# Kernel tuning notes

Measured on AMD Instinct MI355X. Metric: run time of the kernel, lower is better.

## Reference

```python
import jax, jax.numpy as jnp
import numpy as np

N, E, H, NUM_RBF = 50000, 800000, 32, 32
D_IN = 2 * (NUM_RBF + H)  # 128: att_src(H) + att_dst(H) + rbf(2*NUM_RBF)
LN_EPS = 1e-5


def _decompose(t):
    # irreducible decomposition of [..., 3, 3] tensor
    eye = jnp.eye(3, dtype=t.dtype)
    I = jnp.mean(jnp.diagonal(t, axis1=-2, axis2=-1), axis=-1)[..., None, None] * eye
    A = 0.5 * (t - jnp.swapaxes(t, -1, -2))
    S = 0.5 * (t + jnp.swapaxes(t, -1, -2)) - I
    return I, A, S


def _tnorm(t):
    # squared Frobenius norm over last two dims -> [..., H]
    return (t ** 2).sum((-2, -1))


def _chan_lin(t, W):
    # nn.Linear over channel dim: t [N,H,3,3], W [H_out,H_in]
    return jnp.einsum('nhij,gh->ngij', t, W)


def setup_inputs() -> dict:
    key = jax.random.key(0)
    ks = jax.random.split(key, 12)

    def lin(k, o, i):
        return (jax.random.normal(k, (o, i), jnp.float32) / np.sqrt(i)).astype(jnp.float32)

    return {
        'X': jax.random.normal(ks[0], (N, H, 3, 3), jnp.float32),
        'rbf': jax.random.normal(ks[1], (E, 2 * NUM_RBF), jnp.float32),
        'dist': jax.random.uniform(ks[2], (E,), jnp.float32),
        'src': jax.random.randint(ks[3], (E,), 0, N),
        'dst': jax.random.randint(ks[4], (E,), 0, N),
        'Ws0': lin(ks[5], H, D_IN), 'b0': jnp.zeros((H,), jnp.float32),
        'Ws1': lin(ks[6], 2 * H, H), 'b1': jnp.zeros((2 * H,), jnp.float32),
        'Ws2': lin(ks[7], 3 * H, 2 * H), 'b2': jnp.zeros((3 * H,), jnp.float32),
        'Wt': (jax.random.normal(ks[8], (6, H, H), jnp.float32) / np.sqrt(H)).astype(jnp.float32),
        'ln_w': jnp.ones((3 * H,), jnp.float32), 'ln_b': jnp.zeros((3 * H,), jnp.float32),
        'lin_w': lin(ks[9], H, 3 * H), 'lin_b': jnp.zeros((H,), jnp.float32),
    }


def reference(X, rbf, dist, src, dst, Ws0, b0, Ws1, b1, Ws2, b2, Wt, ln_w, ln_b, lin_w, lin_b):
    n = X.shape[0]
    act = jax.nn.silu

    # atom_inf branch: per-node scalar attributes from tensor norms
    I, A, S = _decompose(X)
    x = jnp.concatenate([_tnorm(I), _tnorm(A), _tnorm(S)], axis=-1)  # [N, 3H]
    mu = x.mean(-1, keepdims=True)
    var = x.var(-1, keepdims=True)
    x = (x - mu) / jnp.sqrt(var + LN_EPS) * ln_w + ln_b
    att = act(x @ lin_w.T + lin_b)  # [N, H]

    # edge features: cat(att[src], att[dst], rbf) -> scalar MLP
    e = jnp.concatenate([att[src], att[dst], rbf], axis=-1)  # [E, D_IN]
    e = act(e @ Ws0.T + b0)
    e = act(e @ Ws1.T + b1)
    e = act(e @ Ws2.T + b2)  # [E, 3H]
    C = jnp.ones_like(dist)  # original code overwrites cutoff with ones
    e = (e * C[:, None]).reshape(e.shape[0], H, 3)  # [E, H, 3]

    # normalize node tensors, decompose, per-channel linear mix
    Xn = X / (_tnorm(X) + 1.0)[..., None, None]
    I, A, S = _decompose(Xn)
    I = _chan_lin(I, Wt[0])
    A = _chan_lin(A, Wt[1])
    S = _chan_lin(S, Wt[2])
    Y = I + A + S

    # tensor message passing: gather src, scale by edge factor, scatter-sum to dst
    def mp(T, f):
        return jax.ops.segment_sum(T[src] * f[:, :, None, None], dst, num_segments=n)

    msg = mp(I, e[..., 0]) + mp(A, e[..., 1]) + mp(S, e[..., 2])

    # O(3) group
    B1 = jnp.matmul(msg, Y)
    B2 = jnp.matmul(Y, msg)
    I, A, S = _decompose(B1 + B2)

    normp1 = (_tnorm(I + A + S) + 1.0)[..., None, None]
    I, A, S = I / normp1, A / normp1, S / normp1
    I = _chan_lin(I, Wt[3])
    A = _chan_lin(A, Wt[4])
    S = _chan_lin(S, Wt[5])
    dX = I + A + S
    X_out = Xn + dX + jnp.matmul(dX, dX)  # matrix_power(dX, 2)
    return X_out, e
```

## Files before the change

kernel.cpp:

```cpp
#include <hip/hip_runtime.h>
#include <math.h>

#define HC 32
#define NODE_PER_BLK 8

typedef _Float16 half8 __attribute__((ext_vector_type(8)));
typedef float float4v __attribute__((ext_vector_type(4)));

__device__ __forceinline__ float silu_f(float x) { return x / (1.0f + __expf(-x)); }

__device__ __forceinline__ unsigned int pk2(float a, float b) {
    union { _Float16 h[2]; unsigned int u; } t;
    t.h[0] = (_Float16)a; t.h[1] = (_Float16)b;
    return t.u;
}
__device__ __forceinline__ void unpk2(unsigned int u, float& a, float& b) {
    union { unsigned int u; _Float16 h[2]; } t;
    t.u = u;
    a = (float)t.h[0]; b = (float)t.h[1];
}

__device__ __forceinline__ void recon3(const float* c, float* T) {
    T[0] = c[0] + c[4];  T[1] = c[1] + c[5];  T[2] = c[2] + c[6];
    T[3] = -c[1] + c[5]; T[4] = c[0] + c[7];  T[5] = c[3] + c[8];
    T[6] = -c[2] + c[6]; T[7] = -c[3] + c[8]; T[8] = c[0] - c[4] - c[7];
}

__global__ void prep_weights(const float* __restrict__ Ws0, const float* __restrict__ Ws1,
                             const float* __restrict__ Ws2,
                             _Float16* __restrict__ wf1, _Float16* __restrict__ wf2,
                             _Float16* __restrict__ wf3) {
    int t = blockIdx.x * 256 + threadIdx.x;
    int j = t & 7;
    int lane = (t >> 3) & 63;
    int q = lane >> 4, r = lane & 15;
    if (t < 4096) {
        int fi = t >> 9, kt = fi >> 1, nt = fi & 1;
        wf1[t] = (_Float16)Ws0[(16 * nt + r) * 128 + 32 * kt + 8 * q + j];
    } else if (t < 6144) {
        int t2 = t - 4096;
        int nt = t2 >> 9;
        wf2[t2] = (_Float16)Ws1[(16 * nt + r) * 32 + 8 * q + j];
    } else if (t < 12288) {
        int t3 = t - 6144;
        int fi = t3 >> 9, kt = fi / 6, nt = fi % 6;
        wf3[t3] = (_Float16)Ws2[(16 * nt + r) * 64 + 32 * kt + 8 * q + j];
    }
}

__global__ void hist_kernel(const int* __restrict__ dst, int* __restrict__ cnt, int E) {
    int e = blockIdx.x * 256 + threadIdx.x;
    if (e < E) atomicAdd(&cnt[dst[e]], 1);
}

__global__ __launch_bounds__(1024) void scan_a(const int* __restrict__ cnt,
                                               int* __restrict__ bsum, int N) {
    __shared__ int s[1024];
    int i = blockIdx.x * 1024 + threadIdx.x;
    s[threadIdx.x] = (i < N) ? cnt[i] : 0;
    __syncthreads();
    #pragma unroll
    for (int o = 512; o; o >>= 1) {
        if (threadIdx.x < o) s[threadIdx.x] += s[threadIdx.x + o];
        __syncthreads();
    }
    if (threadIdx.x == 0) bsum[blockIdx.x] = s[0];
}

__global__ __launch_bounds__(1024) void scan_b(int* __restrict__ bsum, int nb) {
    __shared__ int s[1024];
    int v = (threadIdx.x < nb) ? bsum[threadIdx.x] : 0;
    s[threadIdx.x] = v;
    __syncthreads();
    #pragma unroll
    for (int o = 1; o < 1024; o <<= 1) {
        int t = (threadIdx.x >= o) ? s[threadIdx.x - o] : 0;
        __syncthreads();
        s[threadIdx.x] += t;
        __syncthreads();
    }
    if (threadIdx.x < nb) bsum[threadIdx.x] = s[threadIdx.x] - v;
}

__global__ __launch_bounds__(1024) void scan_c(const int* __restrict__ cnt,
                                               const int* __restrict__ bsum,
                                               int* __restrict__ off,
                                               int* __restrict__ cursor, int N) {
    __shared__ int s[1024];
    int i = blockIdx.x * 1024 + threadIdx.x;
    int v = (i < N) ? cnt[i] : 0;
    s[threadIdx.x] = v;
    __syncthreads();
    #pragma unroll
    for (int o = 1; o < 1024; o <<= 1) {
        int t = (threadIdx.x >= o) ? s[threadIdx.x - o] : 0;
        __syncthreads();
        s[threadIdx.x] += t;
        __syncthreads();
    }
    int ex = bsum[blockIdx.x] + s[threadIdx.x] - v;
    if (i < N) {
        off[i] = ex;
        cursor[i] = ex;
        if (i == N - 1) off[N] = ex + v;
    }
}

__global__ void scatter_kernel(const int* __restrict__ src, const int* __restrict__ dst,
                               int* __restrict__ cursor, int2* __restrict__ elist, int E) {
    int e = blockIdx.x * 256 + threadIdx.x;
    if (e >= E) return;
    int d = dst[e];
    int pos = atomicAdd(&cursor[d], 1);
    elist[pos] = make_int2(e, src[e]);
}

__global__ void node_prep(const float* __restrict__ X,
                          const float* __restrict__ lin_w, const float* __restrict__ lin_b,
                          const float* __restrict__ ln_w, const float* __restrict__ ln_b,
                          const float* __restrict__ Wt,
                          float* __restrict__ att, unsigned int* __restrict__ comp_g, int N) {
    __shared__ float sX[NODE_PER_BLK][96];
    __shared__ float sC[NODE_PER_BLK][HC * 9];
    int grp = threadIdx.x >> 5;
    int lane = threadIdx.x & 31;
    int n = blockIdx.x * NODE_PER_BLK + grp;
    bool valid = (n < N);

    float m = 0, a01 = 0, a02 = 0, a12 = 0, s00 = 0, s01 = 0, s02 = 0, s11 = 0, s12 = 0, s22 = 0;
    float tI = 0, tA = 0, tS = 0, tX = 0;
    if (valid) {
        const float* xp = X + (size_t)n * 288 + lane * 9;
        float t00 = xp[0], t01 = xp[1], t02 = xp[2];
        float t10 = xp[3], t11 = xp[4], t12 = xp[5];
        float t20 = xp[6], t21 = xp[7], t22 = xp[8];
        m = (t00 + t11 + t22) * (1.0f / 3.0f);
        a01 = 0.5f * (t01 - t10); a02 = 0.5f * (t02 - t20); a12 = 0.5f * (t12 - t21);
        s00 = t00 - m; s11 = t11 - m; s22 = t22 - m;
        s01 = 0.5f * (t01 + t10); s02 = 0.5f * (t02 + t20); s12 = 0.5f * (t12 + t21);
        tI = 3.0f * m * m;
        tA = 2.0f * (a01 * a01 + a02 * a02 + a12 * a12);
        tS = s00 * s00 + s11 * s11 + s22 * s22 + 2.0f * (s01 * s01 + s02 * s02 + s12 * s12);
        tX = tI + tA + tS;
    }
    float lsum = tI + tA + tS;
    #pragma unroll
    for (int o = 16; o; o >>= 1) lsum += __shfl_xor(lsum, o, 32);
    float mu = lsum * (1.0f / 96.0f);
    float d0 = tI - mu, d1 = tA - mu, d2 = tS - mu;
    float lsq = d0 * d0 + d1 * d1 + d2 * d2;
    #pragma unroll
    for (int o = 16; o; o >>= 1) lsq += __shfl_xor(lsq, o, 32);
    float rstd = rsqrtf(lsq * (1.0f / 96.0f) + 1e-5f);
    if (valid) {
        sX[grp][lane]      = d0 * rstd * ln_w[lane]      + ln_b[lane];
        sX[grp][32 + lane] = d1 * rstd * ln_w[32 + lane] + ln_b[32 + lane];
        sX[grp][64 + lane] = d2 * rstd * ln_w[64 + lane] + ln_b[64 + lane];
    }
    __syncthreads();
    if (valid) {
        float acc = lin_b[lane];
        const float* wr = lin_w + lane * 96;
        #pragma unroll
        for (int k = 0; k < 96; k++) acc += wr[k] * sX[grp][k];
        att[(size_t)n * 32 + lane] = silu_f(acc);
        float inv = 1.0f / (tX + 1.0f);
        float* cc = &sC[grp][lane * 9];
        cc[0] = m * inv;
        cc[1] = a01 * inv; cc[2] = a02 * inv; cc[3] = a12 * inv;
        cc[4] = s00 * inv; cc[5] = s01 * inv; cc[6] = s02 * inv;
        cc[7] = s11 * inv; cc[8] = s12 * inv;
    }
    __syncthreads();
    if (valid) {
        float o[9];
        #pragma unroll
        for (int c = 0; c < 9; c++) o[c] = 0.0f;
        const float* w0 = Wt + lane * 32;
        const float* w1 = Wt + 1024 + lane * 32;
        const float* w2 = Wt + 2048 + lane * 32;
        #pragma unroll
        for (int h = 0; h < 32; h++) {
            float wi = w0[h], wa = w1[h], ws = w2[h];
            const float* ch = &sC[grp][h * 9];
            o[0] += wi * ch[0];
            o[1] += wa * ch[1]; o[2] += wa * ch[2]; o[3] += wa * ch[3];
            o[4] += ws * ch[4]; o[5] += ws * ch[5]; o[6] += ws * ch[6];
            o[7] += ws * ch[7]; o[8] += ws * ch[8];
        }
        unsigned int* cgp = comp_g + (size_t)n * 160 + lane;
        cgp[0]   = pk2(o[0], o[1]);
        cgp[32]  = pk2(o[2], o[3]);
        cgp[64]  = pk2(o[4], o[5]);
        cgp[96]  = pk2(o[6], o[7]);
        cgp[128] = pk2(o[8], 0.0f);
    }
}

__device__ __forceinline__ half8 cvt8v(const float* p) {
    float4 v0 = ((const float4*)p)[0];
    float4 v1 = ((const float4*)p)[1];
    half8 h;
    h[0] = (_Float16)v0.x; h[1] = (_Float16)v0.y; h[2] = (_Float16)v0.z; h[3] = (_Float16)v0.w;
    h[4] = (_Float16)v1.x; h[5] = (_Float16)v1.y; h[6] = (_Float16)v1.z; h[7] = (_Float16)v1.w;
    return h;
}

__global__ __launch_bounds__(256) void edge_mfma(
    const float* __restrict__ att, const float* __restrict__ rbf,
    const int* __restrict__ src, const int* __restrict__ dst,
    const _Float16* __restrict__ wf1, const _Float16* __restrict__ wf2,
    const _Float16* __restrict__ wf3,
    const float* __restrict__ b0, const float* __restrict__ b1, const float* __restrict__ b2,
    float* __restrict__ e_out, int E) {
    __shared__ _Float16 hbuf[4][16][72];
    int w = threadIdx.x >> 6;
    int lane = threadIdx.x & 63;
    int q = lane >> 4, r = lane & 15;
    int ebase = blockIdx.x * 64 + w * 16;
    int er = min(ebase + r, E - 1);
    int s = src[er], d = dst[er];

    half8 a0 = cvt8v(att + (size_t)s * 32 + 8 * q);
    half8 a1 = cvt8v(att + (size_t)d * 32 + 8 * q);
    half8 a2 = cvt8v(rbf + (size_t)er * 64 + 8 * q);
    half8 a3 = cvt8v(rbf + (size_t)er * 64 + 32 + 8 * q);

    const half8* W1 = (const half8*)wf1;
    float bn0 = b0[r], bn1 = b0[16 + r];
    float4v acc10 = {bn0, bn0, bn0, bn0};
    float4v acc11 = {bn1, bn1, bn1, bn1};
    acc10 = __builtin_amdgcn_mfma_f32_16x16x32_f16(a0, W1[0 * 64 + lane], acc10, 0, 0, 0);
    acc11 = __builtin_amdgcn_mfma_f32_16x16x32_f16(a0, W1[1 * 64 + lane], acc11, 0, 0, 0);
    acc10 = __builtin_amdgcn_mfma_f32_16x16x32_f16(a1, W1[2 * 64 + lane], acc10, 0, 0, 0);
    acc11 = __builtin_amdgcn_mfma_f32_16x16x32_f16(a1, W1[3 * 64 + lane], acc11, 0, 0, 0);
    acc10 = __builtin_amdgcn_mfma_f32_16x16x32_f16(a2, W1[4 * 64 + lane], acc10, 0, 0, 0);
    acc11 = __builtin_amdgcn_mfma_f32_16x16x32_f16(a2, W1[5 * 64 + lane], acc11, 0, 0, 0);
    acc10 = __builtin_amdgcn_mfma_f32_16x16x32_f16(a3, W1[6 * 64 + lane], acc10, 0, 0, 0);
    acc11 = __builtin_amdgcn_mfma_f32_16x16x32_f16(a3, W1[7 * 64 + lane], acc11, 0, 0, 0);
    #pragma unroll
    for (int reg = 0; reg < 4; reg++) {
        hbuf[w][4 * q + reg][r]      = (_Float16)silu_f(acc10[reg]);
        hbuf[w][4 * q + reg][16 + r] = (_Float16)silu_f(acc11[reg]);
    }

    half8 ah1 = *(const half8*)&hbuf[w][r][8 * q];
    const half8* W2 = (const half8*)wf2;
    float4v acc2[4];
    #pragma unroll
    for (int nt = 0; nt < 4; nt++) {
        float bb = b1[16 * nt + r];
        acc2[nt] = (float4v){bb, bb, bb, bb};
        acc2[nt] = __builtin_amdgcn_mfma_f32_16x16x32_f16(ah1, W2[nt * 64 + lane], acc2[nt], 0, 0, 0);
    }
    #pragma unroll
    for (int nt = 0; nt < 4; nt++) {
        #pragma unroll
        for (int reg = 0; reg < 4; reg++) {
            hbuf[w][4 * q + reg][16 * nt + r] = (_Float16)silu_f(acc2[nt][reg]);
        }
    }

    half8 ah20 = *(const half8*)&hbuf[w][r][8 * q];
    half8 ah21 = *(const half8*)&hbuf[w][r][32 + 8 * q];
    const half8* W3 = (const half8*)wf3;
    float4v acc3[6];
    #pragma unroll
    for (int nt = 0; nt < 6; nt++) {
        float bb = b2[16 * nt + r];
        acc3[nt] = (float4v){bb, bb, bb, bb};
        acc3[nt] = __builtin_amdgcn_mfma_f32_16x16x32_f16(ah20, W3[nt * 64 + lane], acc3[nt], 0, 0, 0);
        acc3[nt] = __builtin_amdgcn_mfma_f32_16x16x32_f16(ah21, W3[(6 + nt) * 64 + lane], acc3[nt], 0, 0, 0);
    }
    #pragma unroll
    for (int nt = 0; nt < 6; nt++) {
        #pragma unroll
        for (int reg = 0; reg < 4; reg++) {
            int ee = ebase + 4 * q + reg;
            if (ee < E) e_out[(size_t)ee * 96 + 16 * nt + r] = silu_f(acc3[nt][reg]);
        }
    }
}

__global__ __launch_bounds__(256) void gather_final(
    const float* __restrict__ X, const unsigned int* __restrict__ comp_g,
    const float* __restrict__ e_out,
    const int* __restrict__ off, const int2* __restrict__ elist,
    const float* __restrict__ Wt, float* __restrict__ Xout, int N) {
    __shared__ float sB[NODE_PER_BLK][HC * 9];
    int grp = threadIdx.x >> 5;
    int lane = threadIdx.x & 31;
    int n = blockIdx.x * NODE_PER_BLK + grp;
    bool valid = (n < N);

    float cm[9];
    #pragma unroll
    for (int c = 0; c < 9; c++) cm[c] = 0.0f;

    if (valid) {
        int start = off[n], end = off[n + 1];
        int idx = start;
        for (; idx + 4 <= end; idx += 4) {
            int ex[4], sx[4];
            #pragma unroll
            for (int u = 0; u < 4; u++) {
                int2 es = elist[idx + u];
                ex[u] = es.x; sx[u] = es.y;
            }
            float ev[4][3];
            unsigned int cg[4][5];
            #pragma unroll
            for (int u = 0; u < 4; u++) {
                const float* ep = e_out + (size_t)ex[u] * 96 + lane * 3;
                ev[u][0] = ep[0]; ev[u][1] = ep[1]; ev[u][2] = ep[2];
                const unsigned int* cp = comp_g + (size_t)sx[u] * 160 + lane;
                cg[u][0] = cp[0]; cg[u][1] = cp[32]; cg[u][2] = cp[64];
                cg[u][3] = cp[96]; cg[u][4] = cp[128];
            }
            #pragma unroll
            for (int u = 0; u < 4; u++) {
                float c0, c1, c2, c3, c4, c5, c6, c7, c8, cz;
                unpk2(cg[u][0], c0, c1);
                unpk2(cg[u][1], c2, c3);
                unpk2(cg[u][2], c4, c5);
                unpk2(cg[u][3], c6, c7);
                unpk2(cg[u][4], c8, cz);
                float e0 = ev[u][0], e1 = ev[u][1], e2 = ev[u][2];
                cm[0] += e0 * c0;
                cm[1] += e1 * c1; cm[2] += e1 * c2; cm[3] += e1 * c3;
                cm[4] += e2 * c4; cm[5] += e2 * c5; cm[6] += e2 * c6;
                cm[7] += e2 * c7; cm[8] += e2 * c8;
            }
        }
        for (; idx < end; idx++) {
            int2 es = elist[idx];
            const float* ep = e_out + (size_t)es.x * 96 + lane * 3;
            float e0 = ep[0], e1 = ep[1], e2 = ep[2];
            const unsigned int* cp = comp_g + (size_t)es.y * 160 + lane;
            float c0, c1, c2, c3, c4, c5, c6, c7, c8, cz;
            unpk2(cp[0], c0, c1);
            unpk2(cp[32], c2, c3);
            unpk2(cp[64], c4, c5);
            unpk2(cp[96], c6, c7);
            unpk2(cp[128], c8, cz);
            cm[0] += e0 * c0;
            cm[1] += e1 * c1; cm[2] += e1 * c2; cm[3] += e1 * c3;
            cm[4] += e2 * c4; cm[5] += e2 * c5; cm[6] += e2 * c6;
            cm[7] += e2 * c7; cm[8] += e2 * c8;
        }
    }

    if (valid) {
        float cy[9], cz;
        const unsigned int* cgn = comp_g + (size_t)n * 160 + lane;
        unpk2(cgn[0], cy[0], cy[1]);
        unpk2(cgn[32], cy[2], cy[3]);
        unpk2(cgn[64], cy[4], cy[5]);
        unpk2(cgn[96], cy[6], cy[7]);
        unpk2(cgn[128], cy[8], cz);
        float M[9], Y[9];
        recon3(cm, M);
        recon3(cy, Y);
        float B[9];
        #pragma unroll
        for (int i = 0; i < 3; i++) {
            #pragma unroll
            for (int j = 0; j < 3; j++) {
                float acc = 0.0f;
                #pragma unroll
                for (int k = 0; k < 3; k++)
                    acc += M[i * 3 + k] * Y[k * 3 + j] + Y[i * 3 + k] * M[k * 3 + j];
                B[i * 3 + j] = acc;
            }
        }
        float mB = (B[0] + B[4] + B[8]) * (1.0f / 3.0f);
        float tn = 1.0f;
        #pragma unroll
        for (int i = 0; i < 9; i++) tn += B[i] * B[i];
        float itn = 1.0f / tn;
        float* bb = &sB[grp][lane * 9];
        bb[0] = mB * itn;
        bb[1] = 0.5f * (B[1] - B[3]) * itn;
        bb[2] = 0.5f * (B[2] - B[6]) * itn;
        bb[3] = 0.5f * (B[5] - B[7]) * itn;
        bb[4] = (B[0] - mB) * itn;
        bb[5] = 0.5f * (B[1] + B[3]) * itn;
        bb[6] = 0.5f * (B[2] + B[6]) * itn;
        bb[7] = (B[4] - mB) * itn;
        bb[8] = 0.5f * (B[5] + B[7]) * itn;
    }
    __syncthreads();
    if (valid) {
        float o[9];
        #pragma unroll
        for (int c = 0; c < 9; c++) o[c] = 0.0f;
        const float* w3 = Wt + 3 * 1024 + lane * 32;
        const float* w4 = Wt + 4 * 1024 + lane * 32;
        const float* w5 = Wt + 5 * 1024 + lane * 32;
        #pragma unroll
        for (int h = 0; h < 32; h++) {
            float wi = w3[h], wa = w4[h], ws = w5[h];
            const float* ch = &sB[grp][h * 9];
            o[0] += wi * ch[0];
            o[1] += wa * ch[1]; o[2] += wa * ch[2]; o[3] += wa * ch[3];
            o[4] += ws * ch[4]; o[5] += ws * ch[5]; o[6] += ws * ch[6];
            o[7] += ws * ch[7]; o[8] += ws * ch[8];
        }
        float D[9];
        recon3(o, D);
        const float* xp = X + (size_t)n * 288 + lane * 9;
        float xv[9];
        float tt = 0.0f;
        #pragma unroll
        for (int i = 0; i < 9; i++) { xv[i] = xp[i]; tt += xv[i] * xv[i]; }
        float inv = 1.0f / (tt + 1.0f);
        float P[9];
        #pragma unroll
        for (int i = 0; i < 3; i++) {
            #pragma unroll
            for (int j = 0; j < 3; j++) {
                float acc = 0.0f;
                #pragma unroll
                for (int k = 0; k < 3; k++) acc += D[i * 3 + k] * D[k * 3 + j];
                P[i * 3 + j] = acc;
            }
        }
        float* op = Xout + (size_t)n * 288 + lane * 9;
        #pragma unroll
        for (int i = 0; i < 9; i++) op[i] = xv[i] * inv + D[i] + P[i];
    }
}

extern "C" void kernel_launch(void* const* d_in, const int* in_sizes, int n_in,
                              void* d_out, int out_size, void* d_ws, size_t ws_size,
                              hipStream_t stream) {
    const float* X = (const float*)d_in[0];
    const float* rbf = (const float*)d_in[1];
    const int* src = (const int*)d_in[3];
    const int* dst = (const int*)d_in[4];
    const float* Ws0 = (const float*)d_in[5];
    const float* b0 = (const float*)d_in[6];
    const float* Ws1 = (const float*)d_in[7];
    const float* b1 = (const float*)d_in[8];
    const float* Ws2 = (const float*)d_in[9];
    const float* b2 = (const float*)d_in[10];
    const float* Wt = (const float*)d_in[11];
    const float* ln_w = (const float*)d_in[12];
    const float* ln_b = (const float*)d_in[13];
    const float* lin_w = (const float*)d_in[14];
    const float* lin_b = (const float*)d_in[15];

    int N = in_sizes[0] / 288;
    int E = in_sizes[1] / 64;

    float* Xout = (float*)d_out;
    float* e_out = (float*)d_out + (size_t)N * 288;

    float* att = (float*)d_ws;
    unsigned int* comp_g = (unsigned int*)(att + (size_t)N * 32);
    _Float16* wf1 = (_Float16*)(comp_g + (size_t)N * 160);
    _Float16* wf2 = wf1 + 4096;
    _Float16* wf3 = wf2 + 2048;
    int* cnt = (int*)(wf3 + 6144);
    int* off = cnt + N;
    int* cursor = off + N + 1;
    int* bsum = cursor + N + 1;
    int2* elist = (int2*)(bsum + 1026);

    int nb = (N + 1023) / 1024;

    hipMemsetAsync(cnt, 0, (size_t)N * sizeof(int), stream);
    prep_weights<<<48, 256, 0, stream>>>(Ws0, Ws1, Ws2, wf1, wf2, wf3);
    node_prep<<<(N + NODE_PER_BLK - 1) / NODE_PER_BLK, 256, 0, stream>>>(
        X, lin_w, lin_b, ln_w, ln_b, Wt, att, comp_g, N);
    hist_kernel<<<(E + 255) / 256, 256, 0, stream>>>(dst, cnt, E);
    scan_a<<<nb, 1024, 0, stream>>>(cnt, bsum, N);
    scan_b<<<1, 1024, 0, stream>>>(bsum, nb);
    scan_c<<<nb, 1024, 0, stream>>>(cnt, bsum, off, cursor, N);
    scatter_kernel<<<(E + 255) / 256, 256, 0, stream>>>(src, dst, cursor, elist, E);
    edge_mfma<<<(E + 63) / 64, 256, 0, stream>>>(
        att, rbf, src, dst, wf1, wf2, wf3, b0, b1, b2, e_out, E);
    gather_final<<<(N + NODE_PER_BLK - 1) / NODE_PER_BLK, 256, 0, stream>>>(
        X, comp_g, e_out, off, elist, Wt, Xout, N);
}
```

Before: 574.2 us.

## Store att in fp16 and split per-node edge gather across two half-waves

node_prep now writes the attention features as fp16, so edge_mfma loads them directly as half8 vectors with no fp32 load and convert step. This halves the gather traffic for att[src] and att[dst]. gather_final now assigns one 64-lane wavefront per node instead of one 32-lane group, with each half summing half of the incoming edge list. The two partial sums are combined with a cross-half shuffle, and the __syncthreads between the shared-memory write and read is removed because each node's data now stays within a single wavefront. In exchange it costs extra rounding on att, only half the lanes are busy in the epilogue, and there are half as many nodes per block.

```diff
diff --git a/kernel.cpp b/kernel.cpp
--- a/kernel.cpp
+++ b/kernel.cpp
@@ -119,7 +119,7 @@
                           const float* __restrict__ lin_w, const float* __restrict__ lin_b,
                           const float* __restrict__ ln_w, const float* __restrict__ ln_b,
                           const float* __restrict__ Wt,
-                          float* __restrict__ att, unsigned int* __restrict__ comp_g, int N) {
+                          _Float16* __restrict__ att_h, unsigned int* __restrict__ comp_g, int N) {
     __shared__ float sX[NODE_PER_BLK][96];
     __shared__ float sC[NODE_PER_BLK][HC * 9];
     int grp = threadIdx.x >> 5;
@@ -127,7 +127,7 @@
     int n = blockIdx.x * NODE_PER_BLK + grp;
     bool valid = (n < N);
 
-    float m = 0, a01 = 0, a02 = 0, a12 = 0, s00 = 0, s01 = 0, s02 = 0, s11 = 0, s12 = 0, s22 = 0;
+    float m = 0, a01 = 0, a02 = 0, a12 = 0, s00 = 0, s01 = 0, s02 = 0, s11 = 0, s12 = 0;
     float tI = 0, tA = 0, tS = 0, tX = 0;
     if (valid) {
         const float* xp = X + (size_t)n * 288 + lane * 9;
@@ -136,7 +136,7 @@
         float t20 = xp[6], t21 = xp[7], t22 = xp[8];
         m = (t00 + t11 + t22) * (1.0f / 3.0f);
         a01 = 0.5f * (t01 - t10); a02 = 0.5f * (t02 - t20); a12 = 0.5f * (t12 - t21);
-        s00 = t00 - m; s11 = t11 - m; s22 = t22 - m;
+        s00 = t00 - m; s11 = t11 - m; float s22 = t22 - m;
         s01 = 0.5f * (t01 + t10); s02 = 0.5f * (t02 + t20); s12 = 0.5f * (t12 + t21);
         tI = 3.0f * m * m;
         tA = 2.0f * (a01 * a01 + a02 * a02 + a12 * a12);
@@ -163,7 +163,7 @@
         const float* wr = lin_w + lane * 96;
         #pragma unroll
         for (int k = 0; k < 96; k++) acc += wr[k] * sX[grp][k];
-        att[(size_t)n * 32 + lane] = silu_f(acc);
+        att_h[(size_t)n * 32 + lane] = (_Float16)silu_f(acc);
         float inv = 1.0f / (tX + 1.0f);
         float* cc = &sC[grp][lane * 9];
         cc[0] = m * inv;
@@ -207,7 +207,7 @@
 }
 
 __global__ __launch_bounds__(256) void edge_mfma(
-    const float* __restrict__ att, const float* __restrict__ rbf,
+    const _Float16* __restrict__ att_h, const float* __restrict__ rbf,
     const int* __restrict__ src, const int* __restrict__ dst,
     const _Float16* __restrict__ wf1, const _Float16* __restrict__ wf2,
     const _Float16* __restrict__ wf3,
@@ -221,8 +221,8 @@
     int er = min(ebase + r, E - 1);
     int s = src[er], d = dst[er];
 
-    half8 a0 = cvt8v(att + (size_t)s * 32 + 8 * q);
-    half8 a1 = cvt8v(att + (size_t)d * 32 + 8 * q);
+    half8 a0 = ((const half8*)(att_h + (size_t)s * 32))[q];
+    half8 a1 = ((const half8*)(att_h + (size_t)d * 32))[q];
     half8 a2 = cvt8v(rbf + (size_t)er * 64 + 8 * q);
     half8 a3 = cvt8v(rbf + (size_t)er * 64 + 32 + 8 * q);
 
@@ -287,10 +287,12 @@
     const float* __restrict__ e_out,
     const int* __restrict__ off, const int2* __restrict__ elist,
     const float* __restrict__ Wt, float* __restrict__ Xout, int N) {
-    __shared__ float sB[NODE_PER_BLK][HC * 9];
-    int grp = threadIdx.x >> 5;
-    int lane = threadIdx.x & 31;
-    int n = blockIdx.x * NODE_PER_BLK + grp;
+    __shared__ float sB[4][288];
+    int w = threadIdx.x >> 6;
+    int fl = threadIdx.x & 63;
+    int sub = fl >> 5;
+    int lane = fl & 31;
+    int n = blockIdx.x * 4 + w;
     bool valid = (n < N);
 
     float cm[9];
@@ -299,8 +301,11 @@
 
     if (valid) {
         int start = off[n], end = off[n + 1];
-        int idx = start;
-        for (; idx + 4 <= end; idx += 4) {
+        int deg = end - start;
+        int half0 = (deg + 1) >> 1;
+        int idx = start + sub * half0;
+        int stop = sub ? end : start + half0;
+        for (; idx + 4 <= stop; idx += 4) {
             int ex[4], sx[4];
             #pragma unroll
             for (int u = 0; u < 4; u++) {
@@ -332,7 +337,7 @@
                 cm[7] += e2 * c7; cm[8] += e2 * c8;
             }
         }
-        for (; idx < end; idx++) {
+        for (; idx < stop; idx++) {
             int2 es = elist[idx];
             const float* ep = e_out + (size_t)es.x * 96 + lane * 3;
             float e0 = ep[0], e1 = ep[1], e2 = ep[2];
@@ -349,8 +354,10 @@
             cm[7] += e2 * c7; cm[8] += e2 * c8;
         }
     }
-
-    if (valid) {
+    #pragma unroll
+    for (int c = 0; c < 9; c++) cm[c] += __shfl_xor(cm[c], 32, 64);
+
+    if (valid && sub == 0) {
         float cy[9], cz;
         const unsigned int* cgn = comp_g + (size_t)n * 160 + lane;
         unpk2(cgn[0], cy[0], cy[1]);
@@ -378,7 +385,7 @@
         #pragma unroll
         for (int i = 0; i < 9; i++) tn += B[i] * B[i];
         float itn = 1.0f / tn;
-        float* bb = &sB[grp][lane * 9];
+        float* bb = &sB[w][lane * 9];
         bb[0] = mB * itn;
         bb[1] = 0.5f * (B[1] - B[3]) * itn;
         bb[2] = 0.5f * (B[2] - B[6]) * itn;
@@ -388,9 +395,6 @@
         bb[6] = 0.5f * (B[2] + B[6]) * itn;
         bb[7] = (B[4] - mB) * itn;
         bb[8] = 0.5f * (B[5] + B[7]) * itn;
-    }
-    __syncthreads();
-    if (valid) {
         float o[9];
         #pragma unroll
         for (int c = 0; c < 9; c++) o[c] = 0.0f;
@@ -400,7 +404,7 @@
         #pragma unroll
         for (int h = 0; h < 32; h++) {
             float wi = w3[h], wa = w4[h], ws = w5[h];
-            const float* ch = &sB[grp][h * 9];
+            const float* ch = &sB[w][h * 9];
             o[0] += wi * ch[0];
             o[1] += wa * ch[1]; o[2] += wa * ch[2]; o[3] += wa * ch[3];
             o[4] += ws * ch[4]; o[5] += ws * ch[5]; o[6] += ws * ch[6];
@@ -456,8 +460,8 @@
     float* Xout = (float*)d_out;
     float* e_out = (float*)d_out + (size_t)N * 288;
 
-    float* att = (float*)d_ws;
-    unsigned int* comp_g = (unsigned int*)(att + (size_t)N * 32);
+    _Float16* att_h = (_Float16*)d_ws;
+    unsigned int* comp_g = (unsigned int*)(att_h + (size_t)N * 32);
     _Float16* wf1 = (_Float16*)(comp_g + (size_t)N * 160);
     _Float16* wf2 = wf1 + 4096;
     _Float16* wf3 = wf2 + 2048;
@@ -472,14 +476,14 @@
     hipMemsetAsync(cnt, 0, (size_t)N * sizeof(int), stream);
     prep_weights<<<48, 256, 0, stream>>>(Ws0, Ws1, Ws2, wf1, wf2, wf3);
     node_prep<<<(N + NODE_PER_BLK - 1) / NODE_PER_BLK, 256, 0, stream>>>(
-        X, lin_w, lin_b, ln_w, ln_b, Wt, att, comp_g, N);
+        X, lin_w, lin_b, ln_w, ln_b, Wt, att_h, comp_g, N);
     hist_kernel<<<(E + 255) / 256, 256, 0, stream>>>(dst, cnt, E);
     scan_a<<<nb, 1024, 0, stream>>>(cnt, bsum, N);
     scan_b<<<1, 1024, 0, stream>>>(bsum, nb);
     scan_c<<<nb, 1024, 0, stream>>>(cnt, bsum, off, cursor, N);
     scatter_kernel<<<(E + 255) / 256, 256, 0, stream>>>(src, dst, cursor, elist, E);
     edge_mfma<<<(E + 63) / 64, 256, 0, stream>>>(
-        att, rbf, src, dst, wf1, wf2, wf3, b0, b1, b2, e_out, E);
-    gather_final<<<(N + NODE_PER_BLK - 1) / NODE_PER_BLK, 256, 0, stream>>>(
+        att_h, rbf, src, dst, wf1, wf2, wf3, b0, b1, b2, e_out, E);
+    gather_final<<<(N + 3) / 4, 256, 0, stream>>>(
         X, comp_g, e_out, off, elist, Wt, Xout, N);
 }
```

After: 600.5 us. 4.6% more time.
